# Kernel tuning notes

Measured on AMD Instinct MI355X. Metric: run time of the kernel, lower is better.

The kernel has to match this reference:

```python
import jax, jax.numpy as jnp
import numpy as np
from jax import lax

NUM_ITER = 40  # matches init_kwargs num_iter
B, C, H, W = 16, 1, 1024, 1024


def _maxpool2d(x, wh, ww, ph, pw):
    # torch F.max_pool2d with stride 1 and zero-size-preserving padding;
    # padding value is -inf (identity for max), matching torch semantics.
    return lax.reduce_window(
        x, -jnp.inf, lax.max,
        window_dimensions=(1, 1, wh, ww),
        window_strides=(1, 1, 1, 1),
        padding=[(0, 0), (0, 0), (ph, ph), (pw, pw)],
    )


def soft_erode(img):
    # min-pool along H and along W via negated max-pool, then elementwise min
    p1 = -_maxpool2d(-img, 3, 1, 1, 0)
    p2 = -_maxpool2d(-img, 1, 3, 0, 1)
    return jnp.minimum(p1, p2)


def soft_dilate(img):
    return _maxpool2d(img, 3, 3, 1, 1)


def soft_open(img):
    return soft_dilate(soft_erode(img))


def soft_skel(img, num_iter):
    skel = jax.nn.relu(img - soft_open(img))

    def step(carry, _):
        im, sk = carry
        im = soft_erode(im)
        delta = jax.nn.relu(im - soft_open(im))
        sk = sk + jax.nn.relu(delta - sk * delta)
        return (im, sk), None

    (_, skel), _ = lax.scan(step, (img, skel), None, length=num_iter)
    return skel


def setup_inputs() -> dict:
    key = jax.random.key(0)
    img = jax.random.uniform(key, (B, C, H, W), dtype=jnp.float32)
    return {"img": img}


def reference(img):
    return soft_skel(img, NUM_ITER)
```

## Files before the change

kernel.cpp:

```cpp
#include <hip/hip_runtime.h>
#include <math.h>


#define HH 1024
#define WW 1024
#define T 64
#define MTR 11
#define MTC 12
#define RH 86
#define STq 22
#define STRD 88
#define NT 512
#define NIDX 924

#define LD4(p)    (*(const float4*)(p))
#define ST4(p, v) (*(float4*)(p) = (v))

__device__ __forceinline__ float relu_(float x) { return x > 0.f ? x : 0.f; }
__device__ __forceinline__ float4 min4_(float4 a, float4 b) {
    return make_float4(fminf(a.x,b.x), fminf(a.y,b.y), fminf(a.z,b.z), fminf(a.w,b.w));
}
__device__ __forceinline__ float4 max4_(float4 a, float4 b) {
    return make_float4(fmaxf(a.x,b.x), fmaxf(a.y,b.y), fmaxf(a.z,b.z), fmaxf(a.w,b.w));
}
__device__ __forceinline__ float4 hmin4(float L, float4 a, float R) {
    float4 h;
    h.x = fminf(L,   fminf(a.x, a.y)); h.y = fminf(a.x, fminf(a.y, a.z));
    h.z = fminf(a.y, fminf(a.z, a.w)); h.w = fminf(a.z, fminf(a.w, R));
    return h;
}
__device__ __forceinline__ float4 hmax4(float L, float4 a, float R) {
    float4 h;
    h.x = fmaxf(L,   fmaxf(a.x, a.y)); h.y = fmaxf(a.x, fmaxf(a.y, a.z));
    h.z = fmaxf(a.y, fmaxf(a.z, a.w)); h.w = fmaxf(a.z, fmaxf(a.w, R));
    return h;
}
__device__ __forceinline__ float4 dmask4(float4 v, float rm, float4 cm) {
    float4 o;
    o.x = fminf(fminf(v.x, cm.x), rm); o.y = fminf(fminf(v.y, cm.y), rm);
    o.z = fminf(fminf(v.z, cm.z), rm); o.w = fminf(fminf(v.w, cm.w), rm);
    return o;
}
__device__ __forceinline__ void skup(float4& s, float4 e, float4 d, bool init) {
    float4 dl;
    dl.x = relu_(e.x - d.x); dl.y = relu_(e.y - d.y);
    dl.z = relu_(e.z - d.z); dl.w = relu_(e.w - d.w);
    if (init) { s = dl; }
    else {
        s.x += relu_(dl.x - s.x * dl.x); s.y += relu_(dl.y - s.y * dl.y);
        s.z += relu_(dl.z - s.z * dl.z); s.w += relu_(dl.w - s.w * dl.w);
    }
}

__global__ __launch_bounds__(NT, 4) void phase_kernel(
    const float* __restrict__ src, float* __restrict__ dst,
    float* __restrict__ skel, int S, int first, int last)
{
    __shared__ __align__(16) float buf0[RH * STRD + 4];
    __shared__ __align__(16) float buf1[RH * STRD + 4];

    const int h0 = blockIdx.y * T;
    const int w0 = blockIdx.x * T;
    const size_t plane = (size_t)HH * WW;
    const float* sp = src + blockIdx.z * plane;
    float* skp = skel + blockIdx.z * plane;
    float* dp = dst ? dst + blockIdx.z * plane : nullptr;

    const int tid = threadIdx.x;
    const bool border = (h0 == 0) || (w0 == 0) || (h0 + T == HH) || (w0 + T == WW);

    if (!border) {
        const float* base = sp + (size_t)(h0 - MTR) * WW + (w0 - MTC);
        for (int i = tid; i < RH * STq; i += NT) {
            int r = i / STq, q = i - r * STq;
            ST4(&buf0[r * STRD + 4 * q], LD4(base + (size_t)r * WW + 4 * q));
        }
    } else {
        for (int i = tid; i < RH * STRD; i += NT) {
            int r = i / STRD, c = i - r * STRD;
            int gh = h0 - MTR + r, gw = w0 - MTC + c;
            float v = INFINITY;
            if ((unsigned)gh < HH && (unsigned)gw < WW) v = sp[(size_t)gh * WW + gw];
            buf0[r * STRD + c] = v;
        }
    }

    int pq[2], cq[2], oq[2];
    bool act[2], cen[2];
    float4 s0[2], s1[2];
#pragma unroll
    for (int q = 0; q < 2; ++q) {
        int idx = tid + NT * q;
        act[q] = (idx < NIDX);
        int p = idx / STq, c = idx - STq * p;
        pq[q] = p; cq[q] = c;
        oq[q] = (1 + 2 * p) * STRD + 4 * c;
        cen[q] = act[q] && (p >= 5) && (p <= 36) && (c >= 3) && (c <= 18);
    }
    if (!first) {
#pragma unroll
        for (int q = 0; q < 2; ++q) if (cen[q]) {
            const float* g = skp + (size_t)(h0 + 2 * pq[q] - 10) * WW + (w0 + 4 * cq[q] - 12);
            s0[q] = LD4(g); s1[q] = LD4(g + WW);
        }
    }
    __syncthreads();

    for (int t = 1; t <= S + 1; ++t) {
        float* sb = ((t - 1) & 1) ? buf1 : buf0;
        float* db = (t & 1) ? buf1 : buf0;
        const bool do_er = (t <= S);
        const bool do_dl = (t >= 2);
        const bool init = (first != 0) && (t == 2);
#pragma unroll
        for (int q = 0; q < 2; ++q) {
            if (!act[q]) continue;
            const bool cw = cen[q] && do_dl;
            if (!(do_er || cw)) continue;
            const int o = oq[q];
            float4 U   = LD4(sb + o - STRD);
            float4 Am0 = LD4(sb + o - 4);
            float4 A0  = LD4(sb + o);
            float4 Ap0 = LD4(sb + o + 4);
            float4 Am1 = LD4(sb + o + STRD - 4);
            float4 A1  = LD4(sb + o + STRD);
            float4 Ap1 = LD4(sb + o + STRD + 4);
            float4 D   = LD4(sb + o + 2 * STRD);
            float4 ec0, ec1, Um, Up, Dm, Dp;
            if (cw) {
                Um = LD4(sb + o - STRD - 4);
                Up = LD4(sb + o - STRD + 4);
                Dm = LD4(sb + o + 2 * STRD - 4);
                Dp = LD4(sb + o + 2 * STRD + 4);
                ec0 = LD4(db + o);
                ec1 = LD4(db + o + STRD);
            }
            if (do_er) {
                float4 h0q = hmin4(Am0.w, A0, Ap0.x);
                float4 h1q = hmin4(Am1.w, A1, Ap1.x);
                float4 e0 = min4_(min4_(U, A1), h0q);
                float4 e1 = min4_(min4_(A0, D), h1q);
                if (border) {
                    int ghb = h0 - MTR + 1 + 2 * pq[q];
                    int gwb = w0 - MTC + 4 * cq[q];
                    float4 cwm;
                    cwm.x = (unsigned)(gwb + 0) < WW ? -INFINITY : INFINITY;
                    cwm.y = (unsigned)(gwb + 1) < WW ? -INFINITY : INFINITY;
                    cwm.z = (unsigned)(gwb + 2) < WW ? -INFINITY : INFINITY;
                    cwm.w = (unsigned)(gwb + 3) < WW ? -INFINITY : INFINITY;
                    float r0 = (unsigned)ghb       < HH ? -INFINITY : INFINITY;
                    float r1 = (unsigned)(ghb + 1) < HH ? -INFINITY : INFINITY;
                    e0 = max4_(e0, max4_(make_float4(r0, r0, r0, r0), cwm));
                    e1 = max4_(e1, max4_(make_float4(r1, r1, r1, r1), cwm));
                }
                ST4(db + o, e0);
                ST4(db + o + STRD, e1);
            }
            if (cw) {
                float4 tU = U, tA = A0, tB = A1, tD = D;
                float eUm = Um.w, eUp = Up.x, eAm = Am0.w, eAp = Ap0.x;
                float eBm = Am1.w, eBp = Ap1.x, eDm = Dm.w, eDp = Dp.x;
                if (border) {
                    int ghb = h0 - MTR + 1 + 2 * pq[q];
                    int gwb = w0 - MTC + 4 * cq[q];
                    float rm0 = (unsigned)(ghb - 1) < HH ? INFINITY : -INFINITY;
                    float rm1 = (unsigned)(ghb)     < HH ? INFINITY : -INFINITY;
                    float rm2 = (unsigned)(ghb + 1) < HH ? INFINITY : -INFINITY;
                    float rm3 = (unsigned)(ghb + 2) < HH ? INFINITY : -INFINITY;
                    float cmL = (unsigned)(gwb - 1) < WW ? INFINITY : -INFINITY;
                    float cmR = (unsigned)(gwb + 4) < WW ? INFINITY : -INFINITY;
                    float4 cmC;
                    cmC.x = (unsigned)(gwb + 0) < WW ? INFINITY : -INFINITY;
                    cmC.y = (unsigned)(gwb + 1) < WW ? INFINITY : -INFINITY;
                    cmC.z = (unsigned)(gwb + 2) < WW ? INFINITY : -INFINITY;
                    cmC.w = (unsigned)(gwb + 3) < WW ? INFINITY : -INFINITY;
                    tU = dmask4(tU, rm0, cmC); tA = dmask4(tA, rm1, cmC);
                    tB = dmask4(tB, rm2, cmC); tD = dmask4(tD, rm3, cmC);
                    eUm = fminf(fminf(eUm, cmL), rm0); eUp = fminf(fminf(eUp, cmR), rm0);
                    eAm = fminf(fminf(eAm, cmL), rm1); eAp = fminf(fminf(eAp, cmR), rm1);
                    eBm = fminf(fminf(eBm, cmL), rm2); eBp = fminf(fminf(eBp, cmR), rm2);
                    eDm = fminf(fminf(eDm, cmL), rm3); eDp = fminf(fminf(eDp, cmR), rm3);
                }
                float4 hU = hmax4(eUm, tU, eUp);
                float4 hA = hmax4(eAm, tA, eAp);
                float4 hB = hmax4(eBm, tB, eBp);
                float4 hD = hmax4(eDm, tD, eDp);
                float4 d0 = max4_(hU, max4_(hA, hB));
                float4 d1 = max4_(hA, max4_(hB, hD));
                skup(s0[q], ec0, d0, init);
                skup(s1[q], ec1, d1, init);
            }
        }
        __syncthreads();
    }

    const float* eb = (S & 1) ? buf1 : buf0;
#pragma unroll
    for (int q = 0; q < 2; ++q) if (cen[q]) {
        size_t grow = (size_t)(h0 + 2 * pq[q] - 10) * WW + (w0 + 4 * cq[q] - 12);
        ST4(skp + grow, s0[q]);
        ST4(skp + grow + WW, s1[q]);
        if (!last) {
            ST4(dp + grow, LD4(eb + oq[q]));
            ST4(dp + grow + WW, LD4(eb + oq[q] + STRD));
        }
    }
}

extern "C" void kernel_launch(void* const* d_in, const int* in_sizes, int n_in,
                              void* d_out, int out_size, void* d_ws, size_t ws_size,
                              hipStream_t stream) {
    const float* img = (const float*)d_in[0];
    float* skel = (float*)d_out;
    const int B = in_sizes[0] / (HH * WW);
    const size_t plane = (size_t)HH * WW;

    float* e0 = (float*)d_ws;
    float* e1 = e0 + (size_t)B * plane;

    dim3 grid(WW / T, HH / T, B);
    dim3 block(NT);

    const int Ks[5] = {9, 8, 8, 8, 8};
    const float* src = img;
    float* ebufs[2] = {e0, e1};
    for (int p = 0; p < 5; ++p) {
        int first = (p == 0), last = (p == 4);
        float* dstp = last ? nullptr : ebufs[p & 1];
        phase_kernel<<<grid, block, 0, stream>>>(src, dstp, skel, Ks[p], first, last);
        src = dstp;
    }
}
```

Baseline: 989.5 us.

## Give each thread a 4x4 patch instead of two 2x4 patches in shared-memory stencil

Restructures the per-thread work so each thread handles a 4-row by 4-column patch, with one patch per thread instead of two 2x4 patches. This lets vertical neighbour rows be reused across more outputs and replaces float4 side loads with scalar halo loads, cutting LDS traffic per output. The halo is enlarged to 13 rows, the row stride becomes 96, the block grows to 576 threads and the launch-bounds occupancy hint is dropped. The risks are higher register pressure, fewer active threads per patch, and a larger padded tile that adds redundant halo work.

```diff
diff --git a/kernel.cpp b/kernel.cpp
--- a/kernel.cpp
+++ b/kernel.cpp
@@ -5,13 +5,13 @@
 #define HH 1024
 #define WW 1024
 #define T 64
-#define MTR 11
+#define MTR 13
 #define MTC 12
-#define RH 86
-#define STq 22
-#define STRD 88
-#define NT 512
-#define NIDX 924
+#define RH 90
+#define STq 24
+#define STRD 96
+#define NT 576
+#define PADF 4
 
 #define LD4(p)    (*(const float4*)(p))
 #define ST4(p, v) (*(float4*)(p) = (v))
@@ -52,12 +52,14 @@
     }
 }
 
-__global__ __launch_bounds__(NT, 4) void phase_kernel(
+__global__ __launch_bounds__(NT) void phase_kernel(
     const float* __restrict__ src, float* __restrict__ dst,
     float* __restrict__ skel, int S, int first, int last)
 {
-    __shared__ __align__(16) float buf0[RH * STRD + 4];
-    __shared__ __align__(16) float buf1[RH * STRD + 4];
+    __shared__ __align__(16) float b0_[PADF + RH * STRD + PADF];
+    __shared__ __align__(16) float b1_[PADF + RH * STRD + PADF];
+    float* buf0 = b0_ + PADF;
+    float* buf1 = b1_ + PADF;
 
     const int h0 = blockIdx.y * T;
     const int w0 = blockIdx.x * T;
@@ -85,24 +87,17 @@
         }
     }
 
-    int pq[2], cq[2], oq[2];
-    bool act[2], cen[2];
-    float4 s0[2], s1[2];
-#pragma unroll
-    for (int q = 0; q < 2; ++q) {
-        int idx = tid + NT * q;
-        act[q] = (idx < NIDX);
-        int p = idx / STq, c = idx - STq * p;
-        pq[q] = p; cq[q] = c;
-        oq[q] = (1 + 2 * p) * STRD + 4 * c;
-        cen[q] = act[q] && (p >= 5) && (p <= 36) && (c >= 3) && (c <= 18);
-    }
-    if (!first) {
-#pragma unroll
-        for (int q = 0; q < 2; ++q) if (cen[q]) {
-            const float* g = skp + (size_t)(h0 + 2 * pq[q] - 10) * WW + (w0 + 4 * cq[q] - 12);
-            s0[q] = LD4(g); s1[q] = LD4(g + WW);
-        }
+    const int p = tid / STq, c = tid - STq * p;
+    const bool act = (p < 22) && (c < 22);
+    const int o = (1 + 4 * p) * STRD + 4 * c;
+    const bool cen = act && (p >= 3) && (p <= 18) && (c >= 3) && (c <= 18);
+    const int ghb = h0 - MTR + 1 + 4 * p;
+    const int gwb = w0 - MTC + 4 * c;
+
+    float4 s0 = make_float4(0,0,0,0), s1 = s0, s2 = s0, s3 = s0;
+    if (!first && cen) {
+        const float* g = skp + (size_t)ghb * WW + gwb;
+        s0 = LD4(g); s1 = LD4(g + WW); s2 = LD4(g + 2 * WW); s3 = LD4(g + 3 * WW);
     }
     __syncthreads();
 
@@ -112,61 +107,60 @@
         const bool do_er = (t <= S);
         const bool do_dl = (t >= 2);
         const bool init = (first != 0) && (t == 2);
-#pragma unroll
-        for (int q = 0; q < 2; ++q) {
-            if (!act[q]) continue;
-            const bool cw = cen[q] && do_dl;
-            if (!(do_er || cw)) continue;
-            const int o = oq[q];
-            float4 U   = LD4(sb + o - STRD);
-            float4 Am0 = LD4(sb + o - 4);
-            float4 A0  = LD4(sb + o);
-            float4 Ap0 = LD4(sb + o + 4);
-            float4 Am1 = LD4(sb + o + STRD - 4);
-            float4 A1  = LD4(sb + o + STRD);
-            float4 Ap1 = LD4(sb + o + STRD + 4);
-            float4 D   = LD4(sb + o + 2 * STRD);
-            float4 ec0, ec1, Um, Up, Dm, Dp;
+        const bool cw = cen && do_dl;
+        if (act && (do_er || cw)) {
+            float4 U  = LD4(sb + o - STRD);
+            float4 A0 = LD4(sb + o);
+            float4 A1 = LD4(sb + o + STRD);
+            float4 A2 = LD4(sb + o + 2 * STRD);
+            float4 A3 = LD4(sb + o + 3 * STRD);
+            float4 Dq = LD4(sb + o + 4 * STRD);
+            float L0 = sb[o - 1],            R0 = sb[o + 4];
+            float L1 = sb[o + STRD - 1],     R1 = sb[o + STRD + 4];
+            float L2 = sb[o + 2 * STRD - 1], R2 = sb[o + 2 * STRD + 4];
+            float L3 = sb[o + 3 * STRD - 1], R3 = sb[o + 3 * STRD + 4];
+            float4 ec0, ec1, ec2, ec3;
+            float eUL, eUR, eDL, eDR;
             if (cw) {
-                Um = LD4(sb + o - STRD - 4);
-                Up = LD4(sb + o - STRD + 4);
-                Dm = LD4(sb + o + 2 * STRD - 4);
-                Dp = LD4(sb + o + 2 * STRD + 4);
-                ec0 = LD4(db + o);
-                ec1 = LD4(db + o + STRD);
+                eUL = sb[o - STRD - 1];     eUR = sb[o - STRD + 4];
+                eDL = sb[o + 4 * STRD - 1]; eDR = sb[o + 4 * STRD + 4];
+                ec0 = LD4(db + o);              ec1 = LD4(db + o + STRD);
+                ec2 = LD4(db + o + 2 * STRD);   ec3 = LD4(db + o + 3 * STRD);
             }
             if (do_er) {
-                float4 h0q = hmin4(Am0.w, A0, Ap0.x);
-                float4 h1q = hmin4(Am1.w, A1, Ap1.x);
-                float4 e0 = min4_(min4_(U, A1), h0q);
-                float4 e1 = min4_(min4_(A0, D), h1q);
+                float4 e0 = min4_(min4_(U,  A1), hmin4(L0, A0, R0));
+                float4 e1 = min4_(min4_(A0, A2), hmin4(L1, A1, R1));
+                float4 e2 = min4_(min4_(A1, A3), hmin4(L2, A2, R2));
+                float4 e3 = min4_(min4_(A2, Dq), hmin4(L3, A3, R3));
                 if (border) {
-                    int ghb = h0 - MTR + 1 + 2 * pq[q];
-                    int gwb = w0 - MTC + 4 * cq[q];
                     float4 cwm;
                     cwm.x = (unsigned)(gwb + 0) < WW ? -INFINITY : INFINITY;
                     cwm.y = (unsigned)(gwb + 1) < WW ? -INFINITY : INFINITY;
                     cwm.z = (unsigned)(gwb + 2) < WW ? -INFINITY : INFINITY;
                     cwm.w = (unsigned)(gwb + 3) < WW ? -INFINITY : INFINITY;
-                    float r0 = (unsigned)ghb       < HH ? -INFINITY : INFINITY;
+                    float r0 = (unsigned)(ghb + 0) < HH ? -INFINITY : INFINITY;
                     float r1 = (unsigned)(ghb + 1) < HH ? -INFINITY : INFINITY;
+                    float r2 = (unsigned)(ghb + 2) < HH ? -INFINITY : INFINITY;
+                    float r3 = (unsigned)(ghb + 3) < HH ? -INFINITY : INFINITY;
                     e0 = max4_(e0, max4_(make_float4(r0, r0, r0, r0), cwm));
                     e1 = max4_(e1, max4_(make_float4(r1, r1, r1, r1), cwm));
+                    e2 = max4_(e2, max4_(make_float4(r2, r2, r2, r2), cwm));
+                    e3 = max4_(e3, max4_(make_float4(r3, r3, r3, r3), cwm));
                 }
-                ST4(db + o, e0);
-                ST4(db + o + STRD, e1);
+                ST4(db + o, e0);            ST4(db + o + STRD, e1);
+                ST4(db + o + 2 * STRD, e2); ST4(db + o + 3 * STRD, e3);
             }
             if (cw) {
-                float4 tU = U, tA = A0, tB = A1, tD = D;
-                float eUm = Um.w, eUp = Up.x, eAm = Am0.w, eAp = Ap0.x;
-                float eBm = Am1.w, eBp = Ap1.x, eDm = Dm.w, eDp = Dp.x;
+                float4 tU = U, t0 = A0, t1 = A1, t2 = A2, t3 = A3, tD = Dq;
+                float lU = eUL, rU = eUR, l0 = L0, r0s = R0, l1 = L1, r1s = R1;
+                float l2 = L2, r2s = R2, l3 = L3, r3s = R3, lD = eDL, rD = eDR;
                 if (border) {
-                    int ghb = h0 - MTR + 1 + 2 * pq[q];
-                    int gwb = w0 - MTC + 4 * cq[q];
-                    float rm0 = (unsigned)(ghb - 1) < HH ? INFINITY : -INFINITY;
-                    float rm1 = (unsigned)(ghb)     < HH ? INFINITY : -INFINITY;
-                    float rm2 = (unsigned)(ghb + 1) < HH ? INFINITY : -INFINITY;
-                    float rm3 = (unsigned)(ghb + 2) < HH ? INFINITY : -INFINITY;
+                    float rmU = (unsigned)(ghb - 1) < HH ? INFINITY : -INFINITY;
+                    float rm0 = (unsigned)(ghb + 0) < HH ? INFINITY : -INFINITY;
+                    float rm1 = (unsigned)(ghb + 1) < HH ? INFINITY : -INFINITY;
+                    float rm2 = (unsigned)(ghb + 2) < HH ? INFINITY : -INFINITY;
+                    float rm3 = (unsigned)(ghb + 3) < HH ? INFINITY : -INFINITY;
+                    float rmD = (unsigned)(ghb + 4) < HH ? INFINITY : -INFINITY;
                     float cmL = (unsigned)(gwb - 1) < WW ? INFINITY : -INFINITY;
                     float cmR = (unsigned)(gwb + 4) < WW ? INFINITY : -INFINITY;
                     float4 cmC;
@@ -174,35 +168,43 @@
                     cmC.y = (unsigned)(gwb + 1) < WW ? INFINITY : -INFINITY;
                     cmC.z = (unsigned)(gwb + 2) < WW ? INFINITY : -INFINITY;
                     cmC.w = (unsigned)(gwb + 3) < WW ? INFINITY : -INFINITY;
-                    tU = dmask4(tU, rm0, cmC); tA = dmask4(tA, rm1, cmC);
-                    tB = dmask4(tB, rm2, cmC); tD = dmask4(tD, rm3, cmC);
-                    eUm = fminf(fminf(eUm, cmL), rm0); eUp = fminf(fminf(eUp, cmR), rm0);
-                    eAm = fminf(fminf(eAm, cmL), rm1); eAp = fminf(fminf(eAp, cmR), rm1);
-                    eBm = fminf(fminf(eBm, cmL), rm2); eBp = fminf(fminf(eBp, cmR), rm2);
-                    eDm = fminf(fminf(eDm, cmL), rm3); eDp = fminf(fminf(eDp, cmR), rm3);
+                    tU = dmask4(tU, rmU, cmC); t0 = dmask4(t0, rm0, cmC);
+                    t1 = dmask4(t1, rm1, cmC); t2 = dmask4(t2, rm2, cmC);
+                    t3 = dmask4(t3, rm3, cmC); tD = dmask4(tD, rmD, cmC);
+                    lU = fminf(fminf(lU, cmL), rmU); rU = fminf(fminf(rU, cmR), rmU);
+                    l0 = fminf(fminf(l0, cmL), rm0); r0s = fminf(fminf(r0s, cmR), rm0);
+                    l1 = fminf(fminf(l1, cmL), rm1); r1s = fminf(fminf(r1s, cmR), rm1);
+                    l2 = fminf(fminf(l2, cmL), rm2); r2s = fminf(fminf(r2s, cmR), rm2);
+                    l3 = fminf(fminf(l3, cmL), rm3); r3s = fminf(fminf(r3s, cmR), rm3);
+                    lD = fminf(fminf(lD, cmL), rmD); rD = fminf(fminf(rD, cmR), rmD);
                 }
-                float4 hU = hmax4(eUm, tU, eUp);
-                float4 hA = hmax4(eAm, tA, eAp);
-                float4 hB = hmax4(eBm, tB, eBp);
-                float4 hD = hmax4(eDm, tD, eDp);
-                float4 d0 = max4_(hU, max4_(hA, hB));
-                float4 d1 = max4_(hA, max4_(hB, hD));
-                skup(s0[q], ec0, d0, init);
-                skup(s1[q], ec1, d1, init);
+                float4 hU = hmax4(lU, tU, rU);
+                float4 h0 = hmax4(l0, t0, r0s);
+                float4 h1 = hmax4(l1, t1, r1s);
+                float4 h2 = hmax4(l2, t2, r2s);
+                float4 h3 = hmax4(l3, t3, r3s);
+                float4 hD = hmax4(lD, tD, rD);
+                float4 d0 = max4_(hU, max4_(h0, h1));
+                float4 d1 = max4_(h0, max4_(h1, h2));
+                float4 d2 = max4_(h1, max4_(h2, h3));
+                float4 d3 = max4_(h2, max4_(h3, hD));
+                skup(s0, ec0, d0, init); skup(s1, ec1, d1, init);
+                skup(s2, ec2, d2, init); skup(s3, ec3, d3, init);
             }
         }
         __syncthreads();
     }
 
     const float* eb = (S & 1) ? buf1 : buf0;
-#pragma unroll
-    for (int q = 0; q < 2; ++q) if (cen[q]) {
-        size_t grow = (size_t)(h0 + 2 * pq[q] - 10) * WW + (w0 + 4 * cq[q] - 12);
-        ST4(skp + grow, s0[q]);
-        ST4(skp + grow + WW, s1[q]);
+    if (cen) {
+        float* g = skp + (size_t)ghb * WW + gwb;
+        ST4(g, s0); ST4(g + WW, s1); ST4(g + 2 * WW, s2); ST4(g + 3 * WW, s3);
         if (!last) {
-            ST4(dp + grow, LD4(eb + oq[q]));
-            ST4(dp + grow + WW, LD4(eb + oq[q] + STRD));
+            float* gd = dp + (size_t)ghb * WW + gwb;
+            ST4(gd, LD4(eb + o));
+            ST4(gd + WW, LD4(eb + o + STRD));
+            ST4(gd + 2 * WW, LD4(eb + o + 2 * STRD));
+            ST4(gd + 3 * WW, LD4(eb + o + 3 * STRD));
         }
     }
 }
```

Measured after the change: 1.509 ms. 1.53x slower.
